# Performance work log

Hardware: AMD Instinct MI355X
Metric: run time of the kernel (lower is better)

The kernel has to match this reference:

```python
import jax, jax.numpy as jnp
import numpy as np

N = 100000
E = 1600000
D_IN = 128
D_OUT = 128
HEADS = 4
C = D_OUT // HEADS  # per-head channels = 32
NEG_SLOPE = 0.2
EPS_SOFTMAX = 1e-16
EPS_LN = 1e-5


def setup_inputs() -> dict:
    key = jax.random.key(0)
    ks = jax.random.split(key, 10)
    x = jax.random.normal(ks[0], (N, D_IN), dtype=jnp.float32)
    edge_index = jax.random.randint(ks[1], (2, E), 0, N, dtype=jnp.int64)
    s = 1.0 / np.sqrt(D_IN)
    W = jax.random.normal(ks[2], (D_IN, HEADS * C), dtype=jnp.float32) * s
    att_src = jax.random.normal(ks[3], (HEADS, C), dtype=jnp.float32) * (1.0 / np.sqrt(C))
    att_dst = jax.random.normal(ks[4], (HEADS, C), dtype=jnp.float32) * (1.0 / np.sqrt(C))
    gat_bias = jax.random.normal(ks[5], (D_OUT,), dtype=jnp.float32) * 0.02
    skip_W = jax.random.normal(ks[6], (D_IN, D_OUT), dtype=jnp.float32) * s
    skip_b = jax.random.normal(ks[7], (D_OUT,), dtype=jnp.float32) * 0.02
    ln_g = jnp.ones((D_OUT,), dtype=jnp.float32)
    ln_b = jnp.zeros((D_OUT,), dtype=jnp.float32)
    return {"x": x, "edge_index": edge_index, "W": W, "att_src": att_src,
            "att_dst": att_dst, "gat_bias": gat_bias, "skip_W": skip_W,
            "skip_b": skip_b, "ln_g": ln_g, "ln_b": ln_b}


def _gat_edge_conv(x, src, dst, W, att_src, att_dst, gat_bias, skip_W, skip_b, ln_g, ln_b):
    n = x.shape[0]
    h = (x @ W).reshape(n, HEADS, C)                      # [N,H,C]
    a_s = jnp.einsum('nhc,hc->nh', h, att_src)            # [N,H]
    a_d = jnp.einsum('nhc,hc->nh', h, att_dst)            # [N,H]
    e = jax.nn.leaky_relu(a_s[src] + a_d[dst], NEG_SLOPE)  # [E,H]
    # segment softmax over incoming edges of each dst node
    m = jax.ops.segment_max(e, dst, num_segments=n)        # [N,H]
    p = jnp.exp(e - m[dst])
    z = jax.ops.segment_sum(p, dst, num_segments=n)        # [N,H]
    alpha = p / (z[dst] + EPS_SOFTMAX)                     # [E,H]
    msg = h[src] * alpha[:, :, None]                       # [E,H,C]
    out = jax.ops.segment_sum(msg, dst, num_segments=n)    # [N,H,C]
    out = out.reshape(n, HEADS * C) + gat_bias
    out = out + x @ skip_W + skip_b
    mu = out.mean(-1, keepdims=True)
    var = ((out - mu) ** 2).mean(-1, keepdims=True)
    return (out - mu) * jax.lax.rsqrt(var + EPS_LN) * ln_g + ln_b


def reference(x, edge_index, W, att_src, att_dst, gat_bias, skip_W, skip_b, ln_g, ln_b):
    n = x.shape[0]
    loops = jnp.arange(n, dtype=edge_index.dtype)          # PyG GATConv add_self_loops=True
    src = jnp.concatenate([edge_index[0], loops])
    dst = jnp.concatenate([edge_index[1], loops])
    return _gat_edge_conv(x, src, dst, W, att_src, att_dst, gat_bias, skip_W, skip_b, ln_g, ln_b)
```

## Files before the change

### kernel.cpp

```cpp
#include <hip/hip_runtime.h>
#include <hip/hip_bf16.h>

#define D 128
#define HEADS 4
#define NEG_SLOPE 0.2f
#define QSCALE 0.0625f
#define QUNSCALE 16.0f

typedef __attribute__((ext_vector_type(8))) short short8;
typedef __attribute__((ext_vector_type(4))) float f32x4;
typedef __attribute__((ext_vector_type(2))) float f32x2;
typedef __attribute__((ext_vector_type(2))) _Float16 h2;

__device__ __forceinline__ float lrelu(float v) {
    return fmaxf(v, NEG_SLOPE * v);
}

__device__ __forceinline__ short f2bf(float v) {
    __hip_bfloat16 b = __float2bfloat16(v);
    short s;
    __builtin_memcpy(&s, &b, 2);
    return s;
}

__device__ __forceinline__ unsigned short f2h(float v) {
    _Float16 h = (_Float16)v;
    unsigned short s;
    __builtin_memcpy(&s, &h, 2);
    return s;
}

#define BCAP 4608
__global__ __launch_bounds__(256)
void wprep_kernel(const float* __restrict__ W, const float* __restrict__ S,
                  short* __restrict__ wsT, int* __restrict__ woffA, int nb) {
    int idx = blockIdx.x * 256 + threadIdx.x;
    int nn = idx >> 7, k = idx & 127;
    float v = (nn < 128) ? W[k * D + nn] : S[k * D + (nn - 128)];
    wsT[idx] = f2bf(v);
    if (idx < nb) woffA[idx] = idx * BCAP;
}

#define LDSPAD 136
__global__ __launch_bounds__(512, 4)
void gemm_mfma_kernel(const float* __restrict__ x, const short* __restrict__ wsT,
                      const float* __restrict__ skip_b, const float* __restrict__ gat_bias,
                      const float* __restrict__ att_src, const float* __restrict__ att_dst,
                      unsigned short* __restrict__ hb, unsigned short* __restrict__ baseb,
                      float* __restrict__ a_s, float* __restrict__ a_d, int n) {
    __shared__ short xs[64][LDSPAD];
    const int t = threadIdx.x;
    const int row0 = blockIdx.x * 64;
    #pragma unroll
    for (int i = 0; i < 4; ++i) {
        int f = t + 512 * i;
        int row = f >> 5, c4 = (f & 31) * 4;
        float4 v = make_float4(0.f, 0.f, 0.f, 0.f);
        if (row0 + row < n) v = *(const float4*)&x[(size_t)(row0 + row) * D + c4];
        short4 s4;
        s4.x = f2bf(v.x); s4.y = f2bf(v.y); s4.z = f2bf(v.z); s4.w = f2bf(v.w);
        *(short4*)&xs[row][c4] = s4;
    }
    __syncthreads();
    const int wv = t >> 6, lane = t & 63;
    const int lo = lane & 15, hi = lane >> 4;
    const int wr = wv >> 2;
    const int wc = wv & 3;
    f32x4 acc[2][4] = {};
    #pragma unroll
    for (int k0 = 0; k0 < 128; k0 += 32) {
        const int kk = k0 + hi * 8;
        short8 a0 = *(const short8*)&xs[wr * 32 + lo][kk];
        short8 a1 = *(const short8*)&xs[wr * 32 + 16 + lo][kk];
        #pragma unroll
        for (int nt = 0; nt < 4; ++nt) {
            short8 b = *(const short8*)&wsT[(wc * 64 + nt * 16 + lo) * D + kk];
            acc[0][nt] = __builtin_amdgcn_mfma_f32_16x16x32_bf16(a0, b, acc[0][nt], 0, 0, 0);
            acc[1][nt] = __builtin_amdgcn_mfma_f32_16x16x32_bf16(a1, b, acc[1][nt], 0, 0, 0);
        }
    }
    if (wc < 2) {
        float as_[4], ad_[4];
        #pragma unroll
        for (int nt = 0; nt < 4; ++nt) {
            const int c = wc * 64 + nt * 16 + lo;
            as_[nt] = att_src[c];
            ad_[nt] = att_dst[c];
        }
        #pragma unroll
        for (int mt = 0; mt < 2; ++mt) {
            #pragma unroll
            for (int reg = 0; reg < 4; ++reg) {
                float ps0 = acc[mt][0][reg] * as_[0] + acc[mt][1][reg] * as_[1];
                float ps1 = acc[mt][2][reg] * as_[2] + acc[mt][3][reg] * as_[3];
                float pd0 = acc[mt][0][reg] * ad_[0] + acc[mt][1][reg] * ad_[1];
                float pd1 = acc[mt][2][reg] * ad_[2] + acc[mt][3][reg] * ad_[3];
                #pragma unroll
                for (int off = 1; off < 16; off <<= 1) {
                    ps0 += __shfl_xor(ps0, off, 64);
                    ps1 += __shfl_xor(ps1, off, 64);
                    pd0 += __shfl_xor(pd0, off, 64);
                    pd1 += __shfl_xor(pd1, off, 64);
                }
                if (lo == 0) {
                    const int r = row0 + wr * 32 + mt * 16 + hi * 4 + reg;
                    if (r < n) {
                        a_s[r * HEADS + wc * 2 + 0] = ps0;
                        a_s[r * HEADS + wc * 2 + 1] = ps1;
                        a_d[r * HEADS + wc * 2 + 0] = pd0;
                        a_d[r * HEADS + wc * 2 + 1] = pd1;
                    }
                }
            }
        }
    }
    #pragma unroll
    for (int nt = 0; nt < 4; ++nt) {
        const int cc = wc * 64 + nt * 16 + lo;
        const bool isH = cc < 128;
        const float bb = isH ? 0.f : (skip_b[cc - 128] + gat_bias[cc - 128]);
        unsigned short* dst = isH ? hb : baseb;
        const int c = isH ? cc : cc - 128;
        #pragma unroll
        for (int mt = 0; mt < 2; ++mt) {
            const int rbase = row0 + wr * 32 + mt * 16 + hi * 4;
            #pragma unroll
            for (int reg = 0; reg < 4; ++reg) {
                const int r = rbase + reg;
                if (r < n) dst[(size_t)r * D + c] = f2h(acc[mt][nt][reg] + bb);
            }
        }
    }
}

#define BEPT 16
#define BCHUNK (256 * BEPT)

__global__ __launch_bounds__(256)
void binA_kernel(const int* __restrict__ ei, int* __restrict__ woffA,
                 unsigned int* __restrict__ pairs, int E_, int nb) {
    __shared__ int hist[512];
    __shared__ int gbase[512];
    const int t = threadIdx.x;
    for (int q = t; q < 512; q += 256) hist[q] = 0;
    __syncthreads();
    int sv[BEPT], dv[BEPT], rk[BEPT];
    const int base = blockIdx.x * BCHUNK;
    #pragma unroll
    for (int i = 0; i < BEPT; ++i) {
        int e = base + i * 256 + t;
        if (e < E_) {
            sv[i] = ei[e];
            dv[i] = ei[E_ + e];
            rk[i] = atomicAdd(&hist[dv[i] >> 8], 1);
        } else {
            sv[i] = -1;
        }
    }
    __syncthreads();
    for (int q = t; q < nb; q += 256) {
        int v = hist[q];
        gbase[q] = v ? atomicAdd(&woffA[q], v) : 0;
    }
    __syncthreads();
    #pragma unroll
    for (int i = 0; i < BEPT; ++i) {
        if (sv[i] >= 0) {
            int pos = gbase[dv[i] >> 8] + rk[i];
            pairs[pos] = ((unsigned int)sv[i] << 8) | (unsigned int)(dv[i] & 255);
        }
    }
}

#define KCAP 24
__global__ __launch_bounds__(256)
void binB_kernel(const unsigned int* __restrict__ pairs, const int* __restrict__ wcur,
                 int* __restrict__ cnt, int* __restrict__ offs,
                 int* __restrict__ ssrc, int n) {
    __shared__ int nhist[256];
    __shared__ int sc[256];
    __shared__ int nbase[256];
    const int b = blockIdx.x;
    const int t = threadIdx.x;
    const int node0 = b << 8;
    const int sbeg = b * BCAP, send = wcur[b];
    nhist[t] = 0;
    __syncthreads();
    unsigned int pk[KCAP];
    int rk[KCAP];
    int nl = 0;
    for (int e = sbeg + t; e < send; e += 256) {
        unsigned int p = pairs[e];
        int r = atomicAdd(&nhist[p & 255], 1);
        if (nl < KCAP) { pk[nl] = p; rk[nl] = r; }
        ++nl;
    }
    __syncthreads();
    int v = nhist[t];
    sc[t] = v;
    __syncthreads();
    for (int off = 1; off < 256; off <<= 1) {
        int x = (t >= off) ? sc[t - off] : 0;
        __syncthreads();
        sc[t] += x;
        __syncthreads();
    }
    int ex = sc[t] - v;
    nbase[t] = sbeg + ex;
    if (node0 + t < n) {
        cnt[node0 + t] = v;
        offs[node0 + t] = sbeg + ex;
    }
    __syncthreads();
    const int m = nl < KCAP ? nl : KCAP;
    for (int i = 0; i < m; ++i) {
        int pos = nbase[pk[i] & 255] + rk[i];
        ssrc[pos] = (int)(pk[i] >> 8);
    }
}

__global__ __launch_bounds__(256)
void gather_kernel(const int* __restrict__ offs, const int* __restrict__ cnt,
                   const int* __restrict__ ssrc, const float* __restrict__ a_s,
                   const float* __restrict__ a_d, const uint4* __restrict__ hb16,
                   const uint4* __restrict__ baseb16,
                   const float* __restrict__ ln_g, const float* __restrict__ ln_b,
                   float* __restrict__ out, int n) {
    const int lane = threadIdx.x & 63;
    const int i = blockIdx.x * 4 + (threadIdx.x >> 6);
    if (i >= n) return;
    const int e4 = lane >> 2, h4 = lane & 3;
    const int l15 = lane & 15;
    const int grp = lane >> 4;
    const int hh = l15 >> 2;
    const uint4 bv = baseb16[(size_t)i * 16 + l15];
    const float2 g2 = ((const float2*)ln_g)[l15 * 4 + grp];
    const float2 lb2 = ((const float2*)ln_b)[l15 * 4 + grp];
    const float as_h4 = a_s[i * HEADS + h4];
    const float ad_h4 = a_d[i * HEADS + h4];
    const float qself = __expf(lrelu(as_h4 + ad_h4));
    float zacc = (e4 == 0) ? qself : 0.f;
    h2 acc0 = {0.f, 0.f}, acc1 = {0.f, 0.f}, acc2 = {0.f, 0.f}, acc3 = {0.f, 0.f};
    {
        const float qs = __shfl(qself, hh, 64) * QSCALE;
        if (grp == 0) {
            const uint4 u = hb16[(size_t)i * 16 + l15];
            const _Float16 wh = (_Float16)qs;
            const h2 w2 = {wh, wh};
            acc0 = __builtin_bit_cast(h2, u.x) * w2;
            acc1 = __builtin_bit_cast(h2, u.y) * w2;
            acc2 = __builtin_bit_cast(h2, u.z) * w2;
            acc3 = __builtin_bit_cast(h2, u.w) * w2;
        }
    }
    const int o = offs[i];
    const int c = cnt[i];
    for (int k0 = 0; k0 < c; k0 += 16) {
        const int rem = c - k0;
        int srow = 0;
        float q = 0.f;
        if (e4 < rem) {
            const int sidx = ssrc[o + k0 + e4];
            srow = sidx << 4;
            q = __expf(lrelu(a_s[sidx * HEADS + h4] + ad_h4));
        }
        zacc += q;
        const _Float16 qh = (_Float16)(q * QSCALE);
        const h2 qv = {qh, qh};
        const int qpk = __builtin_bit_cast(int, qv);
        const int m = rem < 16 ? rem : 16;
        int ee = 0;
        for (; ee + 8 <= m; ee += 8) {
            const int slA = (ee + grp) << 2;
            const int slB = (ee + 4 + grp) << 2;
            const int rA = __shfl(srow, slA, 64) + l15;
            const int rB = __shfl(srow, slB, 64) + l15;
            const h2 qA = __builtin_bit_cast(h2, __shfl(qpk, slA + hh, 64));
            const h2 qB = __builtin_bit_cast(h2, __shfl(qpk, slB + hh, 64));
            const uint4 uA = hb16[(size_t)(unsigned)rA];
            const uint4 uB = hb16[(size_t)(unsigned)rB];
            acc0 += __builtin_bit_cast(h2, uA.x) * qA;
            acc1 += __builtin_bit_cast(h2, uA.y) * qA;
            acc2 += __builtin_bit_cast(h2, uA.z) * qA;
            acc3 += __builtin_bit_cast(h2, uA.w) * qA;
            acc0 += __builtin_bit_cast(h2, uB.x) * qB;
            acc1 += __builtin_bit_cast(h2, uB.y) * qB;
            acc2 += __builtin_bit_cast(h2, uB.z) * qB;
            acc3 += __builtin_bit_cast(h2, uB.w) * qB;
        }
        for (; ee < m; ee += 4) {
            const int slot = ee + grp;
            const int sl = slot << 2;
            const int rA = __shfl(srow, sl, 64) + l15;
            const h2 qA = __builtin_bit_cast(h2, __shfl(qpk, sl + hh, 64));
            if (slot < m) {
                const uint4 uA = hb16[(size_t)(unsigned)rA];
                acc0 += __builtin_bit_cast(h2, uA.x) * qA;
                acc1 += __builtin_bit_cast(h2, uA.y) * qA;
                acc2 += __builtin_bit_cast(h2, uA.z) * qA;
                acc3 += __builtin_bit_cast(h2, uA.w) * qA;
            }
        }
    }
    #pragma unroll
    for (int off = 16; off < 64; off <<= 1) {
        acc0 += __builtin_bit_cast(h2, __shfl_xor(__builtin_bit_cast(int, acc0), off, 64));
        acc1 += __builtin_bit_cast(h2, __shfl_xor(__builtin_bit_cast(int, acc1), off, 64));
        acc2 += __builtin_bit_cast(h2, __shfl_xor(__builtin_bit_cast(int, acc2), off, 64));
        acc3 += __builtin_bit_cast(h2, __shfl_xor(__builtin_bit_cast(int, acc3), off, 64));
    }
    #pragma unroll
    for (int off = 4; off < 64; off <<= 1) zacc += __shfl_xor(zacc, off, 64);
    const float zz = __shfl(zacc, hh, 64);
    const float rz = QUNSCALE / (zz + 1e-16f);
    const h2 b0 = __builtin_bit_cast(h2, bv.x);
    const h2 b1 = __builtin_bit_cast(h2, bv.y);
    const h2 b2 = __builtin_bit_cast(h2, bv.z);
    const h2 b3 = __builtin_bit_cast(h2, bv.w);
    const float v0 = (float)acc0.x * rz + (float)b0.x;
    const float v1 = (float)acc0.y * rz + (float)b0.y;
    const float v2 = (float)acc1.x * rz + (float)b1.x;
    const float v3 = (float)acc1.y * rz + (float)b1.y;
    const float v4 = (float)acc2.x * rz + (float)b2.x;
    const float v5 = (float)acc2.y * rz + (float)b2.y;
    const float v6 = (float)acc3.x * rz + (float)b3.x;
    const float v7 = (float)acc3.y * rz + (float)b3.y;
    float s1 = v0 + v1 + v2 + v3 + v4 + v5 + v6 + v7;
    float s2 = v0 * v0 + v1 * v1 + v2 * v2 + v3 * v3
             + v4 * v4 + v5 * v5 + v6 * v6 + v7 * v7;
    #pragma unroll
    for (int off = 1; off < 16; off <<= 1) {
        s1 += __shfl_xor(s1, off, 64);
        s2 += __shfl_xor(s2, off, 64);
    }
    const float mu = s1 * (1.f / 128.f);
    const float var = s2 * (1.f / 128.f) - mu * mu;
    const float r = rsqrtf(var + 1e-5f);
    const float lo = grp == 0 ? v0 : grp == 1 ? v2 : grp == 2 ? v4 : v6;
    const float hi = grp == 0 ? v1 : grp == 1 ? v3 : grp == 2 ? v5 : v7;
    f32x2 o2;
    o2.x = (lo - mu) * r * g2.x + lb2.x;
    o2.y = (hi - mu) * r * g2.y + lb2.y;
    __builtin_nontemporal_store(o2, (f32x2*)out + ((size_t)i * 64 + l15 * 4 + grp));
}

extern "C" void kernel_launch(void* const* d_in, const int* in_sizes, int n_in,
                              void* d_out, int out_size, void* d_ws, size_t ws_size,
                              hipStream_t stream) {
    const float* x        = (const float*)d_in[0];
    const int*   ei       = (const int*)d_in[1];
    const float* W        = (const float*)d_in[2];
    const float* att_src  = (const float*)d_in[3];
    const float* att_dst  = (const float*)d_in[4];
    const float* gat_bias = (const float*)d_in[5];
    const float* skip_W   = (const float*)d_in[6];
    const float* skip_b   = (const float*)d_in[7];
    const float* ln_g     = (const float*)d_in[8];
    const float* ln_b     = (const float*)d_in[9];
    float* out = (float*)d_out;

    const int n  = in_sizes[0] / D;
    const int E_ = in_sizes[1] / 2;
    const int nb = (n + 255) >> 8;

    char* p = (char*)d_ws;
    auto carve = [&p](size_t bytes) {
        char* r = p;
        p += (bytes + 255) & ~(size_t)255;
        return r;
    };
    short* wsT            = (short*)carve(32768 * sizeof(short));
    unsigned short* hb    = (unsigned short*)carve((size_t)n * D * 2);
    unsigned short* baseb = (unsigned short*)carve((size_t)n * D * 2);
    float* a_s            = (float*)carve((size_t)n * HEADS * 4);
    float* a_d            = (float*)carve((size_t)n * HEADS * 4);
    int*   cnt            = (int*)carve((size_t)n * 4);
    int*   offs           = (int*)carve((size_t)n * 4);
    int*   woffA          = (int*)carve(512 * 4);
    int*   ssrc           = (int*)carve((size_t)nb * BCAP * 4);
    unsigned int* pairs   = (unsigned int*)carve((size_t)nb * BCAP * 4);

    wprep_kernel<<<128, 256, 0, stream>>>(W, skip_W, wsT, woffA, nb);
    gemm_mfma_kernel<<<(n + 63) / 64, 512, 0, stream>>>(x, wsT, skip_b, gat_bias,
                                                        att_src, att_dst,
                                                        hb, baseb, a_s, a_d, n);
    const int BA = (E_ + BCHUNK - 1) / BCHUNK;
    binA_kernel<<<BA, 256, 0, stream>>>(ei, woffA, pairs, E_, nb);
    binB_kernel<<<nb, 256, 0, stream>>>(pairs, woffA, cnt, offs, ssrc, n);
    gather_kernel<<<(n + 3) / 4, 256, 0, stream>>>(offs, cnt, ssrc, a_s, a_d,
                                                   (const uint4*)hb,
                                                   (const uint4*)baseb,
                                                   ln_g, ln_b, out, n);
}
```

Measured before the change: 284.4 us.

## Stage binning scatters through shared memory for coalesced global writes

Both binning kernels now sort their entries locally in LDS before writing to global memory. binA computes a block-local prefix over the bucket histogram, places the packed pairs into shared arrays grouped by bucket, then streams them out contiguously per bucket. binB writes the per-node-sorted sources into a shared buffer and copies that buffer to ssrc in order. The aim is to replace scattered global stores with coalesced ones, paid for with extra LDS usage (which may lower occupancy), additional barriers, and a prefix scan in binA.

```diff
diff --git a/kernel.cpp b/kernel.cpp
--- a/kernel.cpp
+++ b/kernel.cpp
@@ -140,7 +140,11 @@
 void binA_kernel(const int* __restrict__ ei, int* __restrict__ woffA,
                  unsigned int* __restrict__ pairs, int E_, int nb) {
     __shared__ int hist[512];
+    __shared__ int lbase[512];
     __shared__ int gbase[512];
+    __shared__ int ts[256];
+    __shared__ unsigned int lp[BCHUNK];
+    __shared__ unsigned short lq[BCHUNK];
     const int t = threadIdx.x;
     for (int q = t; q < 512; q += 256) hist[q] = 0;
     __syncthreads();
@@ -158,17 +162,37 @@
         }
     }
     __syncthreads();
+    const int h0 = hist[2 * t], h1 = hist[2 * t + 1];
+    ts[t] = h0 + h1;
+    __syncthreads();
+    for (int off = 1; off < 256; off <<= 1) {
+        int x = (t >= off) ? ts[t - off] : 0;
+        __syncthreads();
+        ts[t] += x;
+        __syncthreads();
+    }
+    const int pb = ts[t] - h0 - h1;
+    lbase[2 * t] = pb;
+    lbase[2 * t + 1] = pb + h0;
     for (int q = t; q < nb; q += 256) {
         int v = hist[q];
         gbase[q] = v ? atomicAdd(&woffA[q], v) : 0;
     }
     __syncthreads();
+    const int total = ts[255];
     #pragma unroll
     for (int i = 0; i < BEPT; ++i) {
         if (sv[i] >= 0) {
-            int pos = gbase[dv[i] >> 8] + rk[i];
-            pairs[pos] = ((unsigned int)sv[i] << 8) | (unsigned int)(dv[i] & 255);
-        }
+            const int q = dv[i] >> 8;
+            const int pos = lbase[q] + rk[i];
+            lp[pos] = ((unsigned int)sv[i] << 8) | (unsigned int)(dv[i] & 255);
+            lq[pos] = (unsigned short)q;
+        }
+    }
+    __syncthreads();
+    for (int i = t; i < total; i += 256) {
+        const int q = lq[i];
+        pairs[gbase[q] + (i - lbase[q])] = lp[i];
     }
 }
 
@@ -179,11 +203,14 @@
                  int* __restrict__ ssrc, int n) {
     __shared__ int nhist[256];
     __shared__ int sc[256];
-    __shared__ int nbase[256];
+    __shared__ int sorted[BCAP];
     const int b = blockIdx.x;
     const int t = threadIdx.x;
     const int node0 = b << 8;
-    const int sbeg = b * BCAP, send = wcur[b];
+    const int sbeg = b * BCAP;
+    int send = wcur[b];
+    if (send > sbeg + BCAP) send = sbeg + BCAP;
+    const int total = send - sbeg;
     nhist[t] = 0;
     __syncthreads();
     unsigned int pk[KCAP];
@@ -196,7 +223,7 @@
         ++nl;
     }
     __syncthreads();
-    int v = nhist[t];
+    const int v = nhist[t];
     sc[t] = v;
     __syncthreads();
     for (int off = 1; off < 256; off <<= 1) {
@@ -205,18 +232,20 @@
         sc[t] += x;
         __syncthreads();
     }
-    int ex = sc[t] - v;
-    nbase[t] = sbeg + ex;
+    const int ex = sc[t] - v;
     if (node0 + t < n) {
         cnt[node0 + t] = v;
         offs[node0 + t] = sbeg + ex;
     }
     __syncthreads();
+    nhist[t] = ex;
+    __syncthreads();
     const int m = nl < KCAP ? nl : KCAP;
     for (int i = 0; i < m; ++i) {
-        int pos = nbase[pk[i] & 255] + rk[i];
-        ssrc[pos] = (int)(pk[i] >> 8);
-    }
+        sorted[nhist[pk[i] & 255] + rk[i]] = (int)(pk[i] >> 8);
+    }
+    __syncthreads();
+    for (int i = t; i < total; i += 256) ssrc[sbeg + i] = sorted[i];
 }
 
 __global__ __launch_bounds__(256)
```

After: 281.8 us. Within noise of the previous version (-0.9%).

## Merge binning kernels with weight prep and GEMM, use finer 64-node buckets

Applied to the files above, without the earlier changes.

Folds the weight-transpose prep into the first binning pass as extra blocks, and runs the second binning pass as extra blocks of the GEMM kernel, cutting five launches to three plus a memset. Buckets shrink from 256 to 64 destination nodes with a smaller per-bucket capacity, so each bucket's local histogram, scan and scatter is lighter and more blocks run in parallel. The fixed per-bucket capacity of 1280 relies on random, near-uniform degrees. Edges past capacity are silently dropped, which is a correctness risk on skewed graphs.

```diff
diff --git a/kernel.cpp b/kernel.cpp
--- a/kernel.cpp
+++ b/kernel.cpp
@@ -7,6 +7,13 @@
 #define QSCALE 0.0625f
 #define QUNSCALE 16.0f
 
+#define BCAP64 1280
+#define NB_HIST 1600
+#define BEPT 16
+#define BCHUNK (256 * BEPT)
+#define WPREP_BLOCKS 128
+#define LDSPAD 136
+
 typedef __attribute__((ext_vector_type(8))) short short8;
 typedef __attribute__((ext_vector_type(4))) float f32x4;
 typedef __attribute__((ext_vector_type(2))) float f32x2;
@@ -30,31 +37,117 @@
     return s;
 }
 
-#define BCAP 4608
 __global__ __launch_bounds__(256)
-void wprep_kernel(const float* __restrict__ W, const float* __restrict__ S,
-                  short* __restrict__ wsT, int* __restrict__ woffA, int nb) {
-    int idx = blockIdx.x * 256 + threadIdx.x;
-    int nn = idx >> 7, k = idx & 127;
-    float v = (nn < 128) ? W[k * D + nn] : S[k * D + (nn - 128)];
-    wsT[idx] = f2bf(v);
-    if (idx < nb) woffA[idx] = idx * BCAP;
-}
-
-#define LDSPAD 136
+void prep_kernel(const float* __restrict__ W, const float* __restrict__ S,
+                 short* __restrict__ wsT,
+                 const int* __restrict__ ei, int* __restrict__ woffA,
+                 unsigned int* __restrict__ pairs, int E_, int nb64, int BA) {
+    const int t = threadIdx.x;
+    if ((int)blockIdx.x >= BA) {
+        const int idx = (blockIdx.x - BA) * 256 + t;
+        const int nn = idx >> 7, k = idx & 127;
+        const float v = (nn < 128) ? W[k * D + nn] : S[k * D + (nn - 128)];
+        wsT[idx] = f2bf(v);
+        return;
+    }
+    __shared__ int hist[NB_HIST];
+    __shared__ int gbase[NB_HIST];
+    for (int q = t; q < nb64; q += 256) hist[q] = 0;
+    __syncthreads();
+    int sv[BEPT], dv[BEPT], rk[BEPT];
+    const int base = blockIdx.x * BCHUNK;
+    #pragma unroll
+    for (int i = 0; i < BEPT; ++i) {
+        const int e = base + i * 256 + t;
+        if (e < E_) {
+            sv[i] = ei[e];
+            dv[i] = ei[E_ + e];
+            rk[i] = atomicAdd(&hist[dv[i] >> 6], 1);
+        } else {
+            sv[i] = -1;
+        }
+    }
+    __syncthreads();
+    for (int q = t; q < nb64; q += 256) {
+        const int v = hist[q];
+        gbase[q] = v ? (q * BCAP64 + atomicAdd(&woffA[q], v)) : 0;
+    }
+    __syncthreads();
+    #pragma unroll
+    for (int i = 0; i < BEPT; ++i) {
+        if (sv[i] >= 0) {
+            const int q = dv[i] >> 6;
+            const unsigned int pos = (unsigned int)(gbase[q] + rk[i]);
+            if (pos < (unsigned int)(q + 1) * BCAP64)
+                pairs[pos] = ((unsigned int)sv[i] << 6) | (unsigned int)(dv[i] & 63);
+        }
+    }
+}
+
 __global__ __launch_bounds__(512, 4)
-void gemm_mfma_kernel(const float* __restrict__ x, const short* __restrict__ wsT,
-                      const float* __restrict__ skip_b, const float* __restrict__ gat_bias,
-                      const float* __restrict__ att_src, const float* __restrict__ att_dst,
-                      unsigned short* __restrict__ hb, unsigned short* __restrict__ baseb,
-                      float* __restrict__ a_s, float* __restrict__ a_d, int n) {
-    __shared__ short xs[64][LDSPAD];
+void mid_kernel(const float* __restrict__ x, const short* __restrict__ wsT,
+                const float* __restrict__ skip_b, const float* __restrict__ gat_bias,
+                const float* __restrict__ att_src, const float* __restrict__ att_dst,
+                unsigned short* __restrict__ hb, unsigned short* __restrict__ baseb,
+                float* __restrict__ a_s, float* __restrict__ a_d,
+                const unsigned int* __restrict__ pairs, const int* __restrict__ wcur,
+                int* __restrict__ cnt, int* __restrict__ offs, int* __restrict__ ssrc,
+                int n, int nb64, int nbbB) {
+    __shared__ __align__(16) char smem[64 * LDSPAD * 2];
     const int t = threadIdx.x;
-    const int row0 = blockIdx.x * 64;
+    if ((int)blockIdx.x < nbbB) {
+        int* lds = (int*)smem;
+        const int sub = t >> 8, tt = t & 255;
+        int* nh = lds + sub * 160;
+        int* sc = lds + sub * 160 + 80;
+        const int qb = blockIdx.x * 2 + sub;
+        const bool valid = qb < nb64;
+        const int sbeg = valid ? qb * BCAP64 : 0;
+        int total = valid ? wcur[qb] : 0;
+        if (total > BCAP64) total = BCAP64;
+        const int send = sbeg + total;
+        if (tt < 64) nh[tt] = 0;
+        __syncthreads();
+        unsigned int pk[6];
+        int rk[6];
+        int nl = 0;
+        #pragma unroll
+        for (int r = 0; r < 5; ++r) {
+            const int e = sbeg + r * 256 + tt;
+            if (e < send) {
+                const unsigned int p = pairs[e];
+                const int rr = atomicAdd(&nh[p & 63], 1);
+                pk[nl] = p; rk[nl] = rr; ++nl;
+            }
+        }
+        __syncthreads();
+        const int v = (tt < 64) ? nh[tt] : 0;
+        if (tt < 64) sc[tt] = v;
+        __syncthreads();
+        for (int off = 1; off < 64; off <<= 1) {
+            const int xv = (tt >= off && tt < 64) ? sc[tt - off] : 0;
+            __syncthreads();
+            if (tt < 64) sc[tt] += xv;
+            __syncthreads();
+        }
+        const int ex = (tt < 64) ? sc[tt] - v : 0;
+        if (tt < 64 && valid) {
+            const int node = qb * 64 + tt;
+            if (node < n) { cnt[node] = v; offs[node] = sbeg + ex; }
+        }
+        __syncthreads();
+        if (tt < 64) nh[tt] = ex;
+        __syncthreads();
+        for (int i = 0; i < nl; ++i)
+            ssrc[sbeg + nh[pk[i] & 63] + rk[i]] = (int)(pk[i] >> 6);
+        return;
+    }
+    short (*xs)[LDSPAD] = (short(*)[LDSPAD])smem;
+    const int row0 = (blockIdx.x - nbbB) * 64;
     #pragma unroll
     for (int i = 0; i < 4; ++i) {
-        int f = t + 512 * i;
-        int row = f >> 5, c4 = (f & 31) * 4;
+        const int f = t + 512 * i;
+        const int row = f >> 5, c4 = (f & 31) * 4;
         float4 v = make_float4(0.f, 0.f, 0.f, 0.f);
         if (row0 + row < n) v = *(const float4*)&x[(size_t)(row0 + row) * D + c4];
         short4 s4;
@@ -130,92 +223,6 @@
                 if (r < n) dst[(size_t)r * D + c] = f2h(acc[mt][nt][reg] + bb);
             }
         }
-    }
-}
-
-#define BEPT 16
-#define BCHUNK (256 * BEPT)
-
-__global__ __launch_bounds__(256)
-void binA_kernel(const int* __restrict__ ei, int* __restrict__ woffA,
-                 unsigned int* __restrict__ pairs, int E_, int nb) {
-    __shared__ int hist[512];
-    __shared__ int gbase[512];
-    const int t = threadIdx.x;
-    for (int q = t; q < 512; q += 256) hist[q] = 0;
-    __syncthreads();
-    int sv[BEPT], dv[BEPT], rk[BEPT];
-    const int base = blockIdx.x * BCHUNK;
-    #pragma unroll
-    for (int i = 0; i < BEPT; ++i) {
-        int e = base + i * 256 + t;
-        if (e < E_) {
-            sv[i] = ei[e];
-            dv[i] = ei[E_ + e];
-            rk[i] = atomicAdd(&hist[dv[i] >> 8], 1);
-        } else {
-            sv[i] = -1;
-        }
-    }
-    __syncthreads();
-    for (int q = t; q < nb; q += 256) {
-        int v = hist[q];
-        gbase[q] = v ? atomicAdd(&woffA[q], v) : 0;
-    }
-    __syncthreads();
-    #pragma unroll
-    for (int i = 0; i < BEPT; ++i) {
-        if (sv[i] >= 0) {
-            int pos = gbase[dv[i] >> 8] + rk[i];
-            pairs[pos] = ((unsigned int)sv[i] << 8) | (unsigned int)(dv[i] & 255);
-        }
-    }
-}
-
-#define KCAP 24
-__global__ __launch_bounds__(256)
-void binB_kernel(const unsigned int* __restrict__ pairs, const int* __restrict__ wcur,
-                 int* __restrict__ cnt, int* __restrict__ offs,
-                 int* __restrict__ ssrc, int n) {
-    __shared__ int nhist[256];
-    __shared__ int sc[256];
-    __shared__ int nbase[256];
-    const int b = blockIdx.x;
-    const int t = threadIdx.x;
-    const int node0 = b << 8;
-    const int sbeg = b * BCAP, send = wcur[b];
-    nhist[t] = 0;
-    __syncthreads();
-    unsigned int pk[KCAP];
-    int rk[KCAP];
-    int nl = 0;
-    for (int e = sbeg + t; e < send; e += 256) {
-        unsigned int p = pairs[e];
-        int r = atomicAdd(&nhist[p & 255], 1);
-        if (nl < KCAP) { pk[nl] = p; rk[nl] = r; }
-        ++nl;
-    }
-    __syncthreads();
-    int v = nhist[t];
-    sc[t] = v;
-    __syncthreads();
-    for (int off = 1; off < 256; off <<= 1) {
-        int x = (t >= off) ? sc[t - off] : 0;
-        __syncthreads();
-        sc[t] += x;
-        __syncthreads();
-    }
-    int ex = sc[t] - v;
-    nbase[t] = sbeg + ex;
-    if (node0 + t < n) {
-        cnt[node0 + t] = v;
-        offs[node0 + t] = sbeg + ex;
-    }
-    __syncthreads();
-    const int m = nl < KCAP ? nl : KCAP;
-    for (int i = 0; i < m; ++i) {
-        int pos = nbase[pk[i] & 255] + rk[i];
-        ssrc[pos] = (int)(pk[i] >> 8);
     }
 }
 
@@ -359,9 +366,10 @@
     const float* ln_b     = (const float*)d_in[9];
     float* out = (float*)d_out;
 
-    const int n  = in_sizes[0] / D;
-    const int E_ = in_sizes[1] / 2;
-    const int nb = (n + 255) >> 8;
+    const int n    = in_sizes[0] / D;
+    const int E_   = in_sizes[1] / 2;
+    const int nb64 = (n + 63) >> 6;
+    const int nbbB = (nb64 + 1) >> 1;
 
     char* p = (char*)d_ws;
     auto carve = [&p](size_t bytes) {
@@ -376,17 +384,21 @@
     float* a_d            = (float*)carve((size_t)n * HEADS * 4);
     int*   cnt            = (int*)carve((size_t)n * 4);
     int*   offs           = (int*)carve((size_t)n * 4);
-    int*   woffA          = (int*)carve(512 * 4);
-    int*   ssrc           = (int*)carve((size_t)nb * BCAP * 4);
-    unsigned int* pairs   = (unsigned int*)carve((size_t)nb * BCAP * 4);
-
-    wprep_kernel<<<128, 256, 0, stream>>>(W, skip_W, wsT, woffA, nb);
-    gemm_mfma_kernel<<<(n + 63) / 64, 512, 0, stream>>>(x, wsT, skip_b, gat_bias,
-                                                        att_src, att_dst,
-                                                        hb, baseb, a_s, a_d, n);
+    int*   woffA          = (int*)carve((size_t)nb64 * 4);
+    int*   ssrc           = (int*)carve((size_t)nb64 * BCAP64 * 4);
+    unsigned int* pairs   = (unsigned int*)carve((size_t)nb64 * BCAP64 * 4);
+
+    hipMemsetAsync(woffA, 0, (size_t)nb64 * 4, stream);
+
     const int BA = (E_ + BCHUNK - 1) / BCHUNK;
-    binA_kernel<<<BA, 256, 0, stream>>>(ei, woffA, pairs, E_, nb);
-    binB_kernel<<<nb, 256, 0, stream>>>(pairs, woffA, cnt, offs, ssrc, n);
+    prep_kernel<<<BA + WPREP_BLOCKS, 256, 0, stream>>>(W, skip_W, wsT, ei, woffA,
+                                                       pairs, E_, nb64, BA);
+    const int ngemm = (n + 63) / 64;
+    mid_kernel<<<nbbB + ngemm, 512, 0, stream>>>(x, wsT, skip_b, gat_bias,
+                                                 att_src, att_dst,
+                                                 hb, baseb, a_s, a_d,
+                                                 pairs, woffA,
+                                                 cnt, offs, ssrc, n, nb64, nbbB);
     gather_kernel<<<(n + 3) / 4, 256, 0, stream>>>(offs, cnt, ssrc, a_s, a_d,
                                                    (const uint4*)hb,
                                                    (const uint4*)baseb,
```

After: 270.7 us. 1.05x faster.
